# Kernel tuning notes

Measured on AMD Instinct MI355X. Metric: run time of the kernel, lower is better.

The kernel has to match this reference:

```python
import jax, jax.numpy as jnp
import numpy as np

N = 8192
D_IN = 128
D_OUT = 128

def setup_inputs() -> dict:
    key = jax.random.key(0)
    k_x, k_q, k_k, k_v = jax.random.split(key, 4)
    scale = 1.0 / np.sqrt(D_IN)
    return {
        "input": jax.random.normal(k_x, (N, D_IN), dtype=jnp.float32),
        # torch Linear weights: [out_features, in_features]
        "Wq": jax.random.normal(k_q, (D_IN, D_IN), dtype=jnp.float32) * scale,
        "Wk": jax.random.normal(k_k, (D_IN, D_IN), dtype=jnp.float32) * scale,
        "Wv": jax.random.normal(k_v, (D_OUT, D_IN), dtype=jnp.float32) * scale,
    }

def reference(input, Wq, Wk, Wv):
    # torch Linear: y = x @ W.T
    Q = input @ Wq.T          # [N, d_in]
    K = input @ Wk.T          # [N, d_in]
    V = input @ Wv.T          # [N, d_out]
    # NOTE: original module has NO 1/sqrt(d) scaling — keep it faithful.
    W = jax.nn.softmax(Q @ K.T, axis=-1)  # [N, N]
    return W @ V              # [N, d_out]
```

## Files before the change

kernel.cpp:

```cpp
#include <hip/hip_runtime.h>
#include <hip/hip_bf16.h>
#include <stdint.h>

#define N_TOK 8192
#define D 128
#define QTILES (N_TOK / 16)
#define KVB 64
#define KVTILES (N_TOK / KVB)
#define LOG2E 1.4426950408889634f

typedef __attribute__((ext_vector_type(8))) short short8;
typedef __attribute__((ext_vector_type(4))) short short4v;
typedef __attribute__((ext_vector_type(4))) float f32x4;
typedef __attribute__((ext_vector_type(8))) _Float16 half8;
typedef __attribute__((ext_vector_type(4))) _Float16 half4;
typedef __attribute__((ext_vector_type(2))) __fp16 fp16x2;

__device__ __forceinline__ f32x4 zero4() {
    f32x4 z; z[0] = 0.f; z[1] = 0.f; z[2] = 0.f; z[3] = 0.f; return z;
}
__device__ __forceinline__ float ex2(float x) {
    return __builtin_amdgcn_exp2f(x);
}
__device__ __forceinline__ float max16(const f32x4* s) {
    float a = fmaxf(fmaxf(s[0][0], s[0][1]), s[0][2]);
    float b = fmaxf(fmaxf(s[0][3], s[1][0]), s[1][1]);
    float c = fmaxf(fmaxf(s[1][2], s[1][3]), s[2][0]);
    float d = fmaxf(fmaxf(s[2][1], s[2][2]), s[2][3]);
    float e = fmaxf(fmaxf(s[3][0], s[3][1]), s[3][2]);
    return fmaxf(fmaxf(fmaxf(a, b), c), fmaxf(fmaxf(d, e), s[3][3]));
}

__global__ void cvt_kernel(const float* __restrict__ Wq, const float* __restrict__ Wk,
                           const float* __restrict__ Wv, ushort* __restrict__ Wf) {
    int i = blockIdx.x * blockDim.x + threadIdx.x;
    int w = i * 4;
    if (w >= 3 * 16384) return;
    int m = w >> 14;
    int off = w & 16383;
    const float* src = (m == 0) ? Wq : ((m == 1) ? Wk : Wv);
    ushort* dst = Wf + (m << 14);
    f32x4 v = *(const f32x4*)(src + off);
    half4 pk;
    #pragma unroll
    for (int r = 0; r < 4; ++r) pk[r] = (_Float16)v[r];
    *(half4*)(dst + off) = pk;
}

__global__ __launch_bounds__(256) void proj_kernel(
    const float* __restrict__ X, const ushort* __restrict__ Wf,
    ushort* __restrict__ Qh, ushort* __restrict__ Kh, ushort* __restrict__ Vt) {
    const int tid = threadIdx.x;
    const int lane = tid & 63;
    const int wid = tid >> 6;
    const int g = lane >> 4, r16 = lane & 15;
    const int qbase = blockIdx.x * 32;

    half8 xf[2][4];
    #pragma unroll
    for (int qa = 0; qa < 2; ++qa) {
        const float* xr = X + (size_t)(qbase + 16 * qa + r16) * D + 8 * g;
        #pragma unroll
        for (int ds = 0; ds < 4; ++ds) {
            f32x4 a = *(const f32x4*)(xr + 32 * ds);
            f32x4 b = *(const f32x4*)(xr + 32 * ds + 4);
            #pragma unroll
            for (int j = 0; j < 4; ++j) {
                xf[qa][ds][j] = (_Float16)a[j];
                xf[qa][ds][4 + j] = (_Float16)b[j];
            }
        }
    }

    #pragma unroll
    for (int m = 0; m < 2; ++m) {
        const ushort* W = Wf + m * 16384;
        ushort* O = m ? Kh : Qh;
        const float sc = m ? 1.0f : LOG2E;
        #pragma unroll
        for (int jj = 0; jj < 2; ++jj) {
            int jt = 2 * wid + jj;
            const ushort* wr = W + (size_t)(16 * jt + r16) * D + 8 * g;
            f32x4 acc[2] = {zero4(), zero4()};
            #pragma unroll
            for (int ds = 0; ds < 4; ++ds) {
                half8 wf = *(const half8*)(wr + 32 * ds);
                #pragma unroll
                for (int qa = 0; qa < 2; ++qa)
                    acc[qa] = __builtin_amdgcn_mfma_f32_16x16x32_f16(wf, xf[qa][ds], acc[qa], 0, 0, 0);
            }
            #pragma unroll
            for (int qa = 0; qa < 2; ++qa) {
                half4 pk;
                #pragma unroll
                for (int r = 0; r < 4; ++r) pk[r] = (_Float16)(acc[qa][r] * sc);
                *(half4*)(O + (size_t)(qbase + 16 * qa + r16) * D + 16 * jt + 4 * g) = pk;
            }
        }
    }
    {
        const ushort* W = Wf + 32768;
        #pragma unroll
        for (int jj = 0; jj < 2; ++jj) {
            int jt = 2 * wid + jj;
            const ushort* wr = W + (size_t)(16 * jt + r16) * D + 8 * g;
            f32x4 acc[2] = {zero4(), zero4()};
            #pragma unroll
            for (int ds = 0; ds < 4; ++ds) {
                half8 wf = *(const half8*)(wr + 32 * ds);
                #pragma unroll
                for (int qa = 0; qa < 2; ++qa)
                    acc[qa] = __builtin_amdgcn_mfma_f32_16x16x32_f16(xf[qa][ds], wf, acc[qa], 0, 0, 0);
            }
            #pragma unroll
            for (int qa = 0; qa < 2; ++qa) {
                half4 pk;
                #pragma unroll
                for (int r = 0; r < 4; ++r) pk[r] = (_Float16)acc[qa][r];
                *(half4*)(Vt + (size_t)(16 * jt + r16) * N_TOK + qbase + 16 * qa + 4 * g) = pk;
            }
        }
    }
}

template<int NS>
__global__ __launch_bounds__(256, 2) void flash_kernel(
    const ushort* __restrict__ Qh, const ushort* __restrict__ Kh,
    const ushort* __restrict__ Vt, ushort* __restrict__ Opb, float* __restrict__ ML) {
    __shared__ __align__(16) ushort K_lds[2][KVB * D];
    __shared__ __align__(16) ushort V_lds[2][D * KVB];
    __shared__ __align__(16) ushort P_lds[4 * 2048];

    const int tid = threadIdx.x;
    const int lane = tid & 63;
    const int wid = tid >> 6;
    const int g = lane >> 4, r16 = lane & 15;
    const int sp = blockIdx.x % NS;
    const int qg = blockIdx.x / NS;
    const int t0 = (KVTILES * sp) / NS;
    const int t1 = (KVTILES * (sp + 1)) / NS;
    const int qbase = qg * 128 + wid * 32;
    const int pswz = (r16 & 7) << 3;

    half8 qf[2][4];
    #pragma unroll
    for (int qa = 0; qa < 2; ++qa) {
        const ushort* qr = Qh + (size_t)(qbase + 16 * qa + r16) * D + 8 * g;
        #pragma unroll
        for (int ds = 0; ds < 4; ++ds)
            qf[qa][ds] = *(const half8*)(qr + 32 * ds);
    }

    float m[2] = {-INFINITY, -INFINITY}, l[2] = {0.f, 0.f};
    f32x4 o[2][8];
    #pragma unroll
    for (int qa = 0; qa < 2; ++qa)
        #pragma unroll
        for (int dt = 0; dt < 8; ++dt) o[qa][dt] = zero4();

    ushort* P_w = &P_lds[wid * 2048];

    short8 sk[4], sv[4];

    auto LOADT = [&](int it) {
        const int kv = it * KVB;
        #pragma unroll
        for (int rr = 0; rr < 4; ++rr) {
            int idx = tid + 256 * rr;
            int row = idx >> 4, seg = idx & 15;
            sk[rr] = *(const short8*)(Kh + (size_t)(kv + row) * D + seg * 8);
        }
        #pragma unroll
        for (int rr = 0; rr < 4; ++rr) {
            int idx = tid + 256 * rr;
            int row = idx >> 3, seg = idx & 7;
            sv[rr] = *(const short8*)(Vt + (size_t)row * N_TOK + kv + seg * 8);
        }
    };
    auto WRITET = [&](int b) {
        #pragma unroll
        for (int rr = 0; rr < 4; ++rr) {
            int idx = tid + 256 * rr;
            int row = idx >> 4, seg = idx & 15;
            *(short8*)&K_lds[b][(row * 128 + seg * 8) ^ ((row & 7) << 3)] = sk[rr];
        }
        #pragma unroll
        for (int rr = 0; rr < 4; ++rr) {
            int idx = tid + 256 * rr;
            int row = idx >> 3, seg = idx & 7;
            *(short8*)&V_lds[b][(row * 64 + seg * 8) ^ ((row & 7) << 3)] = sv[rr];
        }
    };

    LOADT(t0);
    WRITET(0);
    __syncthreads();

    int buf = 0;
    for (int it = t0; it < t1; ++it) {
        if (it + 1 < t1) LOADT(it + 1);

        const ushort* kb = K_lds[buf];
        const ushort* vb = V_lds[buf];

        f32x4 s[2][4];
        #pragma unroll
        for (int qa = 0; qa < 2; ++qa)
            #pragma unroll
            for (int t = 0; t < 4; ++t) s[qa][t] = zero4();
        __builtin_amdgcn_s_setprio(1);
        #pragma unroll
        for (int t = 0; t < 4; ++t) {
            #pragma unroll
            for (int ds = 0; ds < 4; ++ds) {
                int row = 16 * t + r16;
                half8 kf = *(const half8*)&kb[(row * 128 + 32 * ds + 8 * g) ^ ((row & 7) << 3)];
                #pragma unroll
                for (int qa = 0; qa < 2; ++qa)
                    s[qa][t] = __builtin_amdgcn_mfma_f32_16x16x32_f16(kf, qf[qa][ds], s[qa][t], 0, 0, 0);
            }
        }
        __builtin_amdgcn_s_setprio(0);

        #pragma unroll
        for (int qa = 0; qa < 2; ++qa) {
            float tm = max16(s[qa]);
            tm = fmaxf(tm, __shfl_xor(tm, 16));
            tm = fmaxf(tm, __shfl_xor(tm, 32));
            if (!__all(tm <= m[qa])) {
                float mnew = fmaxf(m[qa], tm);
                float scale = ex2(m[qa] - mnew);
                l[qa] *= scale;
                #pragma unroll
                for (int dt = 0; dt < 8; ++dt) o[qa][dt] *= scale;
                m[qa] = mnew;
            }
            float psum = 0.f;
            #pragma unroll
            for (int t = 0; t < 4; ++t) {
                float p0 = ex2(s[qa][t][0] - m[qa]);
                float p1 = ex2(s[qa][t][1] - m[qa]);
                float p2 = ex2(s[qa][t][2] - m[qa]);
                float p3 = ex2(s[qa][t][3] - m[qa]);
                psum += (p0 + p1) + (p2 + p3);
                union { fp16x2 h[2]; short4v s4; } u;
                u.h[0] = __builtin_amdgcn_cvt_pkrtz(p0, p1);
                u.h[1] = __builtin_amdgcn_cvt_pkrtz(p2, p3);
                *(short4v*)&P_w[(qa * 1024 + r16 * 64 + 16 * t + 4 * g) ^ pswz] = u.s4;
            }
            psum += __shfl_xor(psum, 16);
            psum += __shfl_xor(psum, 32);
            l[qa] += psum;
        }

        __builtin_amdgcn_s_setprio(1);
        #pragma unroll
        for (int c = 0; c < 2; ++c) {
            half8 pf0 = *(const half8*)&P_w[(r16 * 64 + 32 * c + 8 * g) ^ pswz];
            half8 pf1 = *(const half8*)&P_w[(1024 + r16 * 64 + 32 * c + 8 * g) ^ pswz];
            #pragma unroll
            for (int dt = 0; dt < 8; ++dt) {
                int row = 16 * dt + r16;
                half8 vf = *(const half8*)&vb[(row * 64 + 32 * c + 8 * g) ^ ((row & 7) << 3)];
                o[0][dt] = __builtin_amdgcn_mfma_f32_16x16x32_f16(vf, pf0, o[0][dt], 0, 0, 0);
                o[1][dt] = __builtin_amdgcn_mfma_f32_16x16x32_f16(vf, pf1, o[1][dt], 0, 0, 0);
            }
        }
        __builtin_amdgcn_s_setprio(0);

        if (it + 1 < t1) WRITET(buf ^ 1);
        __syncthreads();
        buf ^= 1;
    }

    #pragma unroll
    for (int qa = 0; qa < 2; ++qa) {
        ushort* obase = Opb + ((size_t)sp * N_TOK + qbase + 16 * qa + r16) * D + 4 * g;
        #pragma unroll
        for (int dt = 0; dt < 8; ++dt) {
            half4 pk;
            #pragma unroll
            for (int r = 0; r < 4; ++r) pk[r] = (_Float16)o[qa][dt][r];
            *(half4*)(obase + 16 * dt) = pk;
        }
        if (g == 0) {
            int qt = (qbase + 16 * qa) >> 4;
            float* ml = ML + ((size_t)sp * QTILES + qt) * 32;
            ml[r16] = m[qa];
            ml[16 + r16] = l[qa];
        }
    }
}

template<int NS>
__global__ void merge_kernel(const ushort* __restrict__ Opb, const float* __restrict__ ML,
                             float* __restrict__ out) {
    int i = blockIdx.x * blockDim.x + threadIdx.x;
    int e = i * 8;
    if (e >= N_TOK * D) return;
    int q = e >> 7;
    int qt = q >> 4, qr = q & 15;
    float mv[NS], lv[NS];
    float M = -INFINITY;
    #pragma unroll
    for (int s = 0; s < NS; ++s) {
        const float* ml = ML + ((size_t)s * QTILES + qt) * 32;
        mv[s] = ml[qr];
        lv[s] = ml[16 + qr];
        M = fmaxf(M, mv[s]);
    }
    float L = 0.f, a[NS];
    #pragma unroll
    for (int s = 0; s < NS; ++s) { a[s] = __builtin_amdgcn_exp2f(mv[s] - M); L += a[s] * lv[s]; }
    float inv = 1.f / L;
    float acc[8];
    #pragma unroll
    for (int r = 0; r < 8; ++r) acc[r] = 0.f;
    #pragma unroll
    for (int s = 0; s < NS; ++s) {
        half8 ov = *(const half8*)(Opb + (size_t)s * N_TOK * D + e);
        #pragma unroll
        for (int r = 0; r < 8; ++r) acc[r] += (float)ov[r] * a[s];
    }
    f32x4 o0, o1;
    #pragma unroll
    for (int r = 0; r < 4; ++r) { o0[r] = acc[r] * inv; o1[r] = acc[4 + r] * inv; }
    *(f32x4*)(out + e) = o0;
    *(f32x4*)(out + e + 4) = o1;
}

extern "C" void kernel_launch(void* const* d_in, const int* in_sizes, int n_in,
                              void* d_out, int out_size, void* d_ws, size_t ws_size,
                              hipStream_t stream) {
    const float* X  = (const float*)d_in[0];
    const float* Wq = (const float*)d_in[1];
    const float* Wk = (const float*)d_in[2];
    const float* Wv = (const float*)d_in[3];
    float* out = (float*)d_out;

    char* ws = (char*)d_ws;
    ushort* Wf  = (ushort*)(ws);
    ushort* Qh  = (ushort*)(ws + 98304);
    ushort* Kh  = (ushort*)(ws + 2195456);
    ushort* Vt  = (ushort*)(ws + 4292608);
    ushort* Opb = (ushort*)(ws + 6389760);

    const size_t op_off = 6389760;
    const size_t need8 = op_off + (size_t)8 * N_TOK * D * 2 + (size_t)8 * QTILES * 32 * 4;

    cvt_kernel<<<48, 256, 0, stream>>>(Wq, Wk, Wv, Wf);
    proj_kernel<<<256, 256, 0, stream>>>(X, Wf, Qh, Kh, Vt);

    if (ws_size >= need8) {
        float* ML = (float*)(ws + op_off + (size_t)8 * N_TOK * D * 2);
        flash_kernel<8><<<(N_TOK / 128) * 8, 256, 0, stream>>>(Qh, Kh, Vt, Opb, ML);
        merge_kernel<8><<<(N_TOK * D / 8 + 255) / 256, 256, 0, stream>>>(Opb, ML, out);
    } else {
        float* ML = (float*)(ws + op_off + (size_t)4 * N_TOK * D * 2);
        flash_kernel<4><<<(N_TOK / 128) * 4, 256, 0, stream>>>(Qh, Kh, Vt, Opb, ML);
        merge_kernel<4><<<(N_TOK * D / 8 + 255) / 256, 256, 0, stream>>>(Opb, ML, out);
    }
}
```

Measured before the change: 72.72 us.

## Fuse weight conversion into projection kernel and drop setprio hints in flash loop

```diff
diff --git a/kernel.cpp b/kernel.cpp
--- a/kernel.cpp
+++ b/kernel.cpp
@@ -30,25 +30,21 @@
     float e = fmaxf(fmaxf(s[3][0], s[3][1]), s[3][2]);
     return fmaxf(fmaxf(fmaxf(a, b), c), fmaxf(fmaxf(d, e), s[3][3]));
 }
-
-__global__ void cvt_kernel(const float* __restrict__ Wq, const float* __restrict__ Wk,
-                           const float* __restrict__ Wv, ushort* __restrict__ Wf) {
-    int i = blockIdx.x * blockDim.x + threadIdx.x;
-    int w = i * 4;
-    if (w >= 3 * 16384) return;
-    int m = w >> 14;
-    int off = w & 16383;
-    const float* src = (m == 0) ? Wq : ((m == 1) ? Wk : Wv);
-    ushort* dst = Wf + (m << 14);
-    f32x4 v = *(const f32x4*)(src + off);
-    half4 pk;
-    #pragma unroll
-    for (int r = 0; r < 4; ++r) pk[r] = (_Float16)v[r];
-    *(half4*)(dst + off) = pk;
+__device__ __forceinline__ half8 ld_f32_as_h8(const float* p) {
+    f32x4 a = *(const f32x4*)(p);
+    f32x4 b = *(const f32x4*)(p + 4);
+    half8 w;
+    #pragma unroll
+    for (int j = 0; j < 4; ++j) {
+        w[j] = (_Float16)a[j];
+        w[4 + j] = (_Float16)b[j];
+    }
+    return w;
 }
 
 __global__ __launch_bounds__(256) void proj_kernel(
-    const float* __restrict__ X, const ushort* __restrict__ Wf,
+    const float* __restrict__ X, const float* __restrict__ Wq,
+    const float* __restrict__ Wk, const float* __restrict__ Wv,
     ushort* __restrict__ Qh, ushort* __restrict__ Kh, ushort* __restrict__ Vt) {
     const int tid = threadIdx.x;
     const int lane = tid & 63;
@@ -61,30 +57,23 @@
     for (int qa = 0; qa < 2; ++qa) {
         const float* xr = X + (size_t)(qbase + 16 * qa + r16) * D + 8 * g;
         #pragma unroll
-        for (int ds = 0; ds < 4; ++ds) {
-            f32x4 a = *(const f32x4*)(xr + 32 * ds);
-            f32x4 b = *(const f32x4*)(xr + 32 * ds + 4);
-            #pragma unroll
-            for (int j = 0; j < 4; ++j) {
-                xf[qa][ds][j] = (_Float16)a[j];
-                xf[qa][ds][4 + j] = (_Float16)b[j];
-            }
-        }
+        for (int ds = 0; ds < 4; ++ds)
+            xf[qa][ds] = ld_f32_as_h8(xr + 32 * ds);
     }
 
     #pragma unroll
     for (int m = 0; m < 2; ++m) {
-        const ushort* W = Wf + m * 16384;
+        const float* W = m ? Wk : Wq;
         ushort* O = m ? Kh : Qh;
         const float sc = m ? 1.0f : LOG2E;
         #pragma unroll
         for (int jj = 0; jj < 2; ++jj) {
             int jt = 2 * wid + jj;
-            const ushort* wr = W + (size_t)(16 * jt + r16) * D + 8 * g;
+            const float* wr = W + (size_t)(16 * jt + r16) * D + 8 * g;
             f32x4 acc[2] = {zero4(), zero4()};
             #pragma unroll
             for (int ds = 0; ds < 4; ++ds) {
-                half8 wf = *(const half8*)(wr + 32 * ds);
+                half8 wf = ld_f32_as_h8(wr + 32 * ds);
                 #pragma unroll
                 for (int qa = 0; qa < 2; ++qa)
                     acc[qa] = __builtin_amdgcn_mfma_f32_16x16x32_f16(wf, xf[qa][ds], acc[qa], 0, 0, 0);
@@ -99,15 +88,14 @@
         }
     }
     {
-        const ushort* W = Wf + 32768;
         #pragma unroll
         for (int jj = 0; jj < 2; ++jj) {
             int jt = 2 * wid + jj;
-            const ushort* wr = W + (size_t)(16 * jt + r16) * D + 8 * g;
+            const float* wr = Wv + (size_t)(16 * jt + r16) * D + 8 * g;
             f32x4 acc[2] = {zero4(), zero4()};
             #pragma unroll
             for (int ds = 0; ds < 4; ++ds) {
-                half8 wf = *(const half8*)(wr + 32 * ds);
+                half8 wf = ld_f32_as_h8(wr + 32 * ds);
                 #pragma unroll
                 for (int qa = 0; qa < 2; ++qa)
                     acc[qa] = __builtin_amdgcn_mfma_f32_16x16x32_f16(xf[qa][ds], wf, acc[qa], 0, 0, 0);
@@ -208,7 +196,6 @@
         for (int qa = 0; qa < 2; ++qa)
             #pragma unroll
             for (int t = 0; t < 4; ++t) s[qa][t] = zero4();
-        __builtin_amdgcn_s_setprio(1);
         #pragma unroll
         for (int t = 0; t < 4; ++t) {
             #pragma unroll
@@ -220,7 +207,6 @@
                     s[qa][t] = __builtin_amdgcn_mfma_f32_16x16x32_f16(kf, qf[qa][ds], s[qa][t], 0, 0, 0);
             }
         }
-        __builtin_amdgcn_s_setprio(0);
 
         #pragma unroll
         for (int qa = 0; qa < 2; ++qa) {
@@ -253,7 +239,6 @@
             l[qa] += psum;
         }
 
-        __builtin_amdgcn_s_setprio(1);
         #pragma unroll
         for (int c = 0; c < 2; ++c) {
             half8 pf0 = *(const half8*)&P_w[(r16 * 64 + 32 * c + 8 * g) ^ pswz];
@@ -266,7 +251,6 @@
                 o[1][dt] = __builtin_amdgcn_mfma_f32_16x16x32_f16(vf, pf1, o[1][dt], 0, 0, 0);
             }
         }
-        __builtin_amdgcn_s_setprio(0);
 
         if (it + 1 < t1) WRITET(buf ^ 1);
         __syncthreads();
@@ -339,17 +323,15 @@
     float* out = (float*)d_out;
 
     char* ws = (char*)d_ws;
-    ushort* Wf  = (ushort*)(ws);
-    ushort* Qh  = (ushort*)(ws + 98304);
-    ushort* Kh  = (ushort*)(ws + 2195456);
-    ushort* Vt  = (ushort*)(ws + 4292608);
-    ushort* Opb = (ushort*)(ws + 6389760);
-
-    const size_t op_off = 6389760;
+    ushort* Qh  = (ushort*)(ws);
+    ushort* Kh  = (ushort*)(ws + 2097152);
+    ushort* Vt  = (ushort*)(ws + 4194304);
+    ushort* Opb = (ushort*)(ws + 6291456);
+
+    const size_t op_off = 6291456;
     const size_t need8 = op_off + (size_t)8 * N_TOK * D * 2 + (size_t)8 * QTILES * 32 * 4;
 
-    cvt_kernel<<<48, 256, 0, stream>>>(Wq, Wk, Wv, Wf);
-    proj_kernel<<<256, 256, 0, stream>>>(X, Wf, Qh, Kh, Vt);
+    proj_kernel<<<256, 256, 0, stream>>>(X, Wq, Wk, Wv, Qh, Kh, Vt);
 
     if (ws_size >= need8) {
         float* ML = (float*)(ws + op_off + (size_t)8 * N_TOK * D * 2);
```

New measurement: 72.23 us. Within noise of the previous version (-0.7%).
